# Performance work log

Measured on AMD Instinct MI355X. Metric: run time of the kernel, lower is better.

The kernel has to match this reference:

```python
import jax, jax.numpy as jnp
import numpy as np


def setup_inputs() -> dict:
    key0 = jax.random.key(0)
    ks = jax.random.split(key0, 7)
    B, N, M, D, H = 2, 1024, 1024, 256, 128
    s = 1.0 / np.sqrt(D)
    return {
        "query": jax.random.normal(ks[0], (B, N, D), dtype=jnp.float32),
        "key": jax.random.normal(ks[1], (B, M, D), dtype=jnp.float32),
        "Wa_w": jax.random.normal(ks[2], (D, H), dtype=jnp.float32) * s,
        "Wa_b": jax.random.normal(ks[3], (H,), dtype=jnp.float32) * 0.02,
        "Wb_w": jax.random.normal(ks[4], (D, H), dtype=jnp.float32) * s,
        "Wb_b": jax.random.normal(ks[5], (H,), dtype=jnp.float32) * 0.02,
        "v_w": jax.random.normal(ks[6], (H,), dtype=jnp.float32) / np.sqrt(H),
    }


def reference(query, key, Wa_w, Wa_b, Wb_w, Wb_b, v_w):
    # a: [B,N,H], b: [B,M,H]
    a = query @ Wa_w + Wa_b
    b = key @ Wb_w + Wb_b
    # scores: tanh of broadcast add [B,N,M,H], contracted with v -> [B,N,M]
    scores = jnp.einsum("bnmh,h->bnm", jnp.tanh(a[:, :, None, :] + b[:, None, :, :]), v_w)
    attn = jax.nn.softmax(scores, axis=-1)
    # attended: [B,N,D]
    return jnp.einsum("bnm,bmd->bnd", attn, key)
```

## Files before the change

kernel.cpp:

```cpp
#include <hip/hip_runtime.h>
#include <hip/hip_fp16.h>

#define BB 2
#define NN 1024
#define MM 1024
#define DD 256
#define HH 128
#define C2LE 2.8853900817779268f
#define NEG2LOG2E -2.8853900817779268f
#define SHIFT_C -4.3280860f

typedef float v2f __attribute__((ext_vector_type(2)));
typedef float v4f __attribute__((ext_vector_type(4)));
typedef _Float16 h8 __attribute__((ext_vector_type(8)));

__global__ __launch_bounds__(256) void proj_conv_kernel(
    const float* __restrict__ query, const float* __restrict__ key,
    const float* __restrict__ Wa_w, const float* __restrict__ Wa_b,
    const float* __restrict__ Wb_w, const float* __restrict__ Wb_b,
    float* __restrict__ EaT, float* __restrict__ Eb,
    __half* __restrict__ KT_hi) {
    __shared__ float rows[8][DD];
    __shared__ float partial[8][HH];
    __shared__ float t[64][65];
    const int tid = threadIdx.x;

    if (blockIdx.x >= 512) {
        const int cid = blockIdx.x - 512;
        const int m0 = (cid & 15) * 64, d0 = ((cid >> 4) & 3) * 64, b = cid >> 6;
        for (int i = tid; i < 1024; i += 256) {
            const int r = i >> 4, c4 = i & 15;
            const float4 v =
                *(const float4*)&key[((size_t)(b * MM + m0 + r)) * DD + d0 + c4 * 4];
            t[r][c4 * 4 + 0] = v.x; t[r][c4 * 4 + 1] = v.y;
            t[r][c4 * 4 + 2] = v.z; t[r][c4 * 4 + 3] = v.w;
        }
        __syncthreads();
        for (int i = tid; i < 4096; i += 256) {
            const int dr = i >> 6, mc = i & 63;
            KT_hi[((size_t)(b * DD + d0 + dr)) * MM + m0 + mc] =
                __float2half(t[mc][dr]);
        }
        return;
    }

    const int rb = blockIdx.x * 8;
    const bool isA = rb < BB * NN;
    const float* in = isA ? query : key;
    const float* W  = isA ? Wa_w : Wb_w;
    const float* bias = isA ? Wa_b : Wb_b;
    const int base = isA ? rb : rb - BB * NN;

    const float4* in4 = (const float4*)(in + (size_t)base * DD);
    float4* rows4 = (float4*)rows;
    rows4[tid] = in4[tid];
    rows4[tid + 256] = in4[tid + 256];
    __syncthreads();

    const int h = tid & 127, half = tid >> 7;
    const int d0 = half * 128;
    float acc[8] = {};
    for (int d = d0; d < d0 + 128; d += 4) {
        const float w0 = W[(d + 0) * HH + h];
        const float w1 = W[(d + 1) * HH + h];
        const float w2 = W[(d + 2) * HH + h];
        const float w3 = W[(d + 3) * HH + h];
#pragma unroll
        for (int r = 0; r < 8; ++r) {
            const float4 rv = *(const float4*)&rows[r][d];
            acc[r] = fmaf(rv.x, w0, fmaf(rv.y, w1, fmaf(rv.z, w2, fmaf(rv.w, w3, acc[r]))));
        }
    }
    if (half) {
#pragma unroll
        for (int r = 0; r < 8; ++r) partial[r][h] = acc[r];
    }
    __syncthreads();
    if (!half) {
        const float bv = bias[h];
        float ev[8];
#pragma unroll
        for (int r = 0; r < 8; ++r)
            ev[r] = __builtin_amdgcn_exp2f(C2LE * (acc[r] + partial[r][h] + bv));
        if (isA) {
            const int bq = base >> 10, nb = base & (NN - 1);
            float* dst = EaT + ((size_t)(bq * HH + h)) * NN + nb;
            *(float4*)dst = *(float4*)&ev[0];
            *(float4*)(dst + 4) = *(float4*)&ev[4];
        } else {
#pragma unroll
            for (int r = 0; r < 8; ++r)
                Eb[(size_t)(base + r) * HH + h] = ev[r];
        }
    }
}

__global__ __launch_bounds__(256) void scores_kernel(
    const float* __restrict__ EaT, const float* __restrict__ Eb,
    const float* __restrict__ v_w, __half* __restrict__ Ph,
    float* __restrict__ psum) {
    __shared__ float b_s[128 * 64];
    __shared__ float a_s[64 * 32];
    const int tid = threadIdx.x;
    const int m0 = blockIdx.x * 128, n0 = blockIdx.y * 32, b = blockIdx.z;
    const int lane = tid & 63;
    const int ng = __builtin_amdgcn_readfirstlane(threadIdx.x >> 6);
    const int skey = lane & 15;

    v2f acc[2][4] = {};
    for (int hc = 0; hc < 2; ++hc) {
        __syncthreads();
        for (int i = tid; i < 128 * 16; i += 256) {
            const int r = i >> 4, h4 = i & 15;
            *(float4*)&b_s[r * 64 + ((h4 ^ (r & 15)) << 2)] =
                *(const float4*)&Eb[((size_t)(b * MM + m0 + r)) * HH + hc * 64 + h4 * 4];
        }
        for (int i = tid; i < 64 * 8; i += 256) {
            const int hh = i >> 3, n4 = i & 7;
            *(float4*)&a_s[hh * 32 + n4 * 4] =
                *(const float4*)&EaT[((size_t)(b * HH + hc * 64 + hh)) * NN + n0 + n4 * 4];
        }
        __syncthreads();

#pragma unroll 4
        for (int h4 = 0; h4 < 16; ++h4) {
            const float4 w4 = *(const float4*)&v_w[hc * 64 + h4 * 4];
            const float* ap = &a_s[h4 * 4 * 32 + ng * 8];
            v2f A0[4], A1[4], A2[4], A3[4];
#pragma unroll
            for (int np = 0; np < 4; ++np) {
                A0[np] = *(const v2f*)&ap[0 * 32 + np * 2];
                A1[np] = *(const v2f*)&ap[1 * 32 + np * 2];
                A2[np] = *(const v2f*)&ap[2 * 32 + np * 2];
                A3[np] = *(const v2f*)&ap[3 * 32 + np * 2];
            }
#pragma unroll
            for (int mt = 0; mt < 2; ++mt) {
                const float4 b4 = *(const float4*)
                    &b_s[(mt * 64 + lane) * 64 + ((h4 ^ skey) << 2)];
#pragma unroll
                for (int np = 0; np < 4; ++np) {
                    const v2f u0 = A0[np] * b4.x + 1.0f;
                    const v2f u1 = A1[np] * b4.y + 1.0f;
                    const v2f u2 = A2[np] * b4.z + 1.0f;
                    const v2f u3 = A3[np] * b4.w + 1.0f;
                    const v2f p01 = u0 * u1, p23 = u2 * u3;
                    const v2f An = w4.x * u1 + w4.y * u0;
                    const v2f Bn = w4.z * u3 + w4.w * u2;
                    const v2f num = An * p23 + Bn * p01;
                    const v2f Pp = p01 * p23;
                    v2f r2;
                    r2.x = __builtin_amdgcn_rcpf(Pp.x);
                    r2.y = __builtin_amdgcn_rcpf(Pp.y);
                    acc[mt][np] = num * r2 + acc[mt][np];
                }
            }
        }
    }

    const size_t prow = ((size_t)b * NN + n0 + ng * 8) * MM + m0 + lane;
#pragma unroll
    for (int j = 0; j < 8; ++j) {
#pragma unroll
        for (int mt = 0; mt < 2; ++mt) {
            const float pv = __builtin_amdgcn_exp2f(
                fmaf(acc[mt][j >> 1][j & 1], NEG2LOG2E, SHIFT_C));
            Ph[prow + (size_t)j * MM + mt * 64] = __float2half(pv);
            float s = pv;
#pragma unroll
            for (int o = 32; o > 0; o >>= 1) s += __shfl_xor(s, o);
            if (lane == 0)
                psum[((size_t)(m0 / 64 + mt) * BB + b) * NN + n0 + ng * 8 + j] = s;
        }
    }
}

__global__ __launch_bounds__(512) void attend_kernel(
    const __half* __restrict__ Ph, const __half* __restrict__ KT_hi,
    float* __restrict__ partial) {
    __shared__ __align__(16) __half Ab[2][4096];
    __shared__ __align__(16) __half Bh[2][4096];

    const int bid = blockIdx.x;
    const int xcd = bid & 7, idx = bid >> 3;
    const int b = idx & 1, ks = (idx >> 1) & 3, dt = (idx >> 3) & 3;
    const int nt = xcd * 2 + ((idx >> 5) & 1);
    const int n0 = nt * 64, d0 = dt * 64, m0 = ks * 256;

    const int tid = threadIdx.x;
    const int lane = tid & 63;
    const int srow = tid & 15, skg = (tid >> 4) & 3;
    const int ssub = tid >> 6, skh = ssub & 1, st = ssub >> 1;
    const int scol = m0 + skh * 32 + skg * 8;

    const __half* srcA = Ph    + ((size_t)(b * NN + n0 + st * 16 + srow)) * MM + scol;
    const __half* srcB = KT_hi + ((size_t)(b * DD + d0 + st * 16 + srow)) * MM + scol;

    const int wave = __builtin_amdgcn_readfirstlane(threadIdx.x >> 6);
    const int t0 = (wave >> 2) * 2, td = wave & 3;

    v4f c0 = {0.f, 0.f, 0.f, 0.f}, c1 = c0;

    h8 ra = *(const h8*)srcA;
    h8 rb = *(const h8*)srcB;

    int cur = 0;
#pragma unroll 1
    for (int step = 0; step < 4; ++step) {
        *(h8*)&Ab[cur][tid * 8] = ra;
        *(h8*)&Bh[cur][tid * 8] = rb;
        if (step < 3) {
            ra = *(const h8*)(srcA + (step + 1) * 64);
            rb = *(const h8*)(srcB + (step + 1) * 64);
        }
        asm volatile("s_waitcnt lgkmcnt(0)" ::: "memory");
        __builtin_amdgcn_sched_barrier(0);
        __builtin_amdgcn_s_barrier();

        const __half* A = Ab[cur];
        const __half* B = Bh[cur];
        const h8 a00 = *(const h8*)&A[((t0 * 2 + 0) * 64 + lane) * 8];
        const h8 a01 = *(const h8*)&A[((t0 * 2 + 1) * 64 + lane) * 8];
        const h8 a10 = *(const h8*)&A[((t0 * 2 + 2) * 64 + lane) * 8];
        const h8 a11 = *(const h8*)&A[((t0 * 2 + 3) * 64 + lane) * 8];
        const h8 b0  = *(const h8*)&B[((td * 2 + 0) * 64 + lane) * 8];
        const h8 b1  = *(const h8*)&B[((td * 2 + 1) * 64 + lane) * 8];
        c0 = __builtin_amdgcn_mfma_f32_16x16x32_f16(a00, b0, c0, 0, 0, 0);
        c0 = __builtin_amdgcn_mfma_f32_16x16x32_f16(a01, b1, c0, 0, 0, 0);
        c1 = __builtin_amdgcn_mfma_f32_16x16x32_f16(a10, b0, c1, 0, 0, 0);
        c1 = __builtin_amdgcn_mfma_f32_16x16x32_f16(a11, b1, c1, 0, 0, 0);
        cur ^= 1;
    }

    const int row16 = lane & 15, kg = lane >> 4;
    float* pp0 = partial +
        (((size_t)ks * BB + b) * NN + n0 + t0 * 16 + kg * 4) * DD + d0 + td * 16 + row16;
    float* pp1 = pp0 + (size_t)16 * DD;
#pragma unroll
    for (int r = 0; r < 4; ++r) pp0[(size_t)r * DD] = c0[r];
#pragma unroll
    for (int r = 0; r < 4; ++r) pp1[(size_t)r * DD] = c1[r];
}

__global__ __launch_bounds__(256) void combine_kernel(
    const float* __restrict__ partial, const float* __restrict__ psum,
    float* __restrict__ out) {
    const int n = blockIdx.x, b = blockIdx.y, d = threadIdx.x;
    float s = 0.f;
#pragma unroll
    for (int q = 0; q < 16; ++q)
        s += psum[((size_t)q * BB + b) * NN + n];
    const size_t off = ((size_t)b * NN + n) * DD + d;
    float a = 0.f;
#pragma unroll
    for (int ks = 0; ks < 4; ++ks)
        a += partial[((size_t)ks * BB) * NN * DD + off];
    out[off] = a * __builtin_amdgcn_rcpf(s);
}

extern "C" void kernel_launch(void* const* d_in, const int* in_sizes, int n_in,
                              void* d_out, int out_size, void* d_ws, size_t ws_size,
                              hipStream_t stream) {
    const float* query = (const float*)d_in[0];
    const float* key   = (const float*)d_in[1];
    const float* Wa_w  = (const float*)d_in[2];
    const float* Wa_b  = (const float*)d_in[3];
    const float* Wb_w  = (const float*)d_in[4];
    const float* Wb_b  = (const float*)d_in[5];
    const float* v_w   = (const float*)d_in[6];
    float* out = (float*)d_out;

    float* ws = (float*)d_ws;
    float* EaT  = ws;
    float* Eb   = EaT + BB * NN * HH;
    float* psum = Eb + BB * MM * HH;
    __half* Ph    = (__half*)(psum + 16 * BB * NN);
    __half* KT_hi = Ph + (size_t)BB * NN * MM;
    float* partial = (float*)(KT_hi + (size_t)BB * DD * MM);

    proj_conv_kernel<<<dim3(512 + 128), dim3(256), 0, stream>>>(
        query, key, Wa_w, Wa_b, Wb_w, Wb_b, EaT, Eb, KT_hi);
    scores_kernel<<<dim3(MM / 128, NN / 32, BB), dim3(256), 0, stream>>>(
        EaT, Eb, v_w, Ph, psum);
    attend_kernel<<<dim3(512), dim3(512), 0, stream>>>(
        Ph, KT_hi, partial);
    combine_kernel<<<dim3(NN, BB), dim3(256), 0, stream>>>(
        partial, psum, out);
}
```

Measured before the change: 58.31 us.

## Fuse combine into attend kernel by removing split-K over M

```diff
diff --git a/kernel.cpp b/kernel.cpp
--- a/kernel.cpp
+++ b/kernel.cpp
@@ -177,85 +177,74 @@
 
 __global__ __launch_bounds__(512) void attend_kernel(
     const __half* __restrict__ Ph, const __half* __restrict__ KT_hi,
-    float* __restrict__ partial) {
-    __shared__ __align__(16) __half Ab[2][4096];
-    __shared__ __align__(16) __half Bh[2][4096];
+    const float* __restrict__ psum, float* __restrict__ out) {
+    __shared__ __align__(16) __half Ab[2][4 * 512];
+    __shared__ __align__(16) __half Bb[2][8 * 512];
+    __shared__ float inv[32];
 
     const int bid = blockIdx.x;
-    const int xcd = bid & 7, idx = bid >> 3;
-    const int b = idx & 1, ks = (idx >> 1) & 3, dt = (idx >> 3) & 3;
-    const int nt = xcd * 2 + ((idx >> 5) & 1);
-    const int n0 = nt * 64, d0 = dt * 64, m0 = ks * 256;
+    const int g = bid & 7, nt = bid >> 3;
+    const int dt = g >> 1, b = g & 1;
+    const int n0 = nt * 32, d0 = dt * 64;
 
     const int tid = threadIdx.x;
     const int lane = tid & 63;
-    const int srow = tid & 15, skg = (tid >> 4) & 3;
-    const int ssub = tid >> 6, skh = ssub & 1, st = ssub >> 1;
-    const int scol = m0 + skh * 32 + skg * 8;
-
-    const __half* srcA = Ph    + ((size_t)(b * NN + n0 + st * 16 + srow)) * MM + scol;
-    const __half* srcB = KT_hi + ((size_t)(b * DD + d0 + st * 16 + srow)) * MM + scol;
+    const int row16 = lane & 15, kg = lane >> 4;
+
+    if (tid < 32) {
+        float s = 0.f;
+#pragma unroll
+        for (int q = 0; q < 16; ++q)
+            s += psum[((size_t)q * BB + b) * NN + n0 + tid];
+        inv[tid] = __builtin_amdgcn_rcpf(s);
+    }
+
+    const int cb = tid >> 6;
+    const int sdB = cb >> 1, skhB = cb & 1;
+    const __half* srcB = KT_hi +
+        ((size_t)(b * DD + d0 + sdB * 16 + row16)) * MM + skhB * 32 + kg * 8;
+    const bool hasA = tid < 256;
+    const int ca = cb & 3;
+    const int snA = ca >> 1, skhA = ca & 1;
+    const __half* srcA = Ph +
+        ((size_t)(b * NN + n0 + snA * 16 + row16)) * MM + skhA * 32 + kg * 8;
 
     const int wave = __builtin_amdgcn_readfirstlane(threadIdx.x >> 6);
-    const int t0 = (wave >> 2) * 2, td = wave & 3;
-
-    v4f c0 = {0.f, 0.f, 0.f, 0.f}, c1 = c0;
-
-    h8 ra = *(const h8*)srcA;
+    const int t = wave >> 2, td = wave & 3;
+
+    v4f c = {0.f, 0.f, 0.f, 0.f};
+
     h8 rb = *(const h8*)srcB;
+    h8 ra;
+    if (hasA) ra = *(const h8*)srcA;
 
     int cur = 0;
 #pragma unroll 1
-    for (int step = 0; step < 4; ++step) {
-        *(h8*)&Ab[cur][tid * 8] = ra;
-        *(h8*)&Bh[cur][tid * 8] = rb;
-        if (step < 3) {
-            ra = *(const h8*)(srcA + (step + 1) * 64);
+    for (int step = 0; step < 16; ++step) {
+        *(h8*)&Bb[cur][cb * 512 + lane * 8] = rb;
+        if (hasA) *(h8*)&Ab[cur][ca * 512 + lane * 8] = ra;
+        if (step < 15) {
             rb = *(const h8*)(srcB + (step + 1) * 64);
+            if (hasA) ra = *(const h8*)(srcA + (step + 1) * 64);
         }
         asm volatile("s_waitcnt lgkmcnt(0)" ::: "memory");
         __builtin_amdgcn_sched_barrier(0);
         __builtin_amdgcn_s_barrier();
 
-        const __half* A = Ab[cur];
-        const __half* B = Bh[cur];
-        const h8 a00 = *(const h8*)&A[((t0 * 2 + 0) * 64 + lane) * 8];
-        const h8 a01 = *(const h8*)&A[((t0 * 2 + 1) * 64 + lane) * 8];
-        const h8 a10 = *(const h8*)&A[((t0 * 2 + 2) * 64 + lane) * 8];
-        const h8 a11 = *(const h8*)&A[((t0 * 2 + 3) * 64 + lane) * 8];
-        const h8 b0  = *(const h8*)&B[((td * 2 + 0) * 64 + lane) * 8];
-        const h8 b1  = *(const h8*)&B[((td * 2 + 1) * 64 + lane) * 8];
-        c0 = __builtin_amdgcn_mfma_f32_16x16x32_f16(a00, b0, c0, 0, 0, 0);
-        c0 = __builtin_amdgcn_mfma_f32_16x16x32_f16(a01, b1, c0, 0, 0, 0);
-        c1 = __builtin_amdgcn_mfma_f32_16x16x32_f16(a10, b0, c1, 0, 0, 0);
-        c1 = __builtin_amdgcn_mfma_f32_16x16x32_f16(a11, b1, c1, 0, 0, 0);
+        const h8 a0 = *(const h8*)&Ab[cur][(t * 2 + 0) * 512 + lane * 8];
+        const h8 a1 = *(const h8*)&Ab[cur][(t * 2 + 1) * 512 + lane * 8];
+        const h8 b0 = *(const h8*)&Bb[cur][(td * 2 + 0) * 512 + lane * 8];
+        const h8 b1 = *(const h8*)&Bb[cur][(td * 2 + 1) * 512 + lane * 8];
+        c = __builtin_amdgcn_mfma_f32_16x16x32_f16(a0, b0, c, 0, 0, 0);
+        c = __builtin_amdgcn_mfma_f32_16x16x32_f16(a1, b1, c, 0, 0, 0);
         cur ^= 1;
     }
 
-    const int row16 = lane & 15, kg = lane >> 4;
-    float* pp0 = partial +
-        (((size_t)ks * BB + b) * NN + n0 + t0 * 16 + kg * 4) * DD + d0 + td * 16 + row16;
-    float* pp1 = pp0 + (size_t)16 * DD;
-#pragma unroll
-    for (int r = 0; r < 4; ++r) pp0[(size_t)r * DD] = c0[r];
-#pragma unroll
-    for (int r = 0; r < 4; ++r) pp1[(size_t)r * DD] = c1[r];
-}
-
-__global__ __launch_bounds__(256) void combine_kernel(
-    const float* __restrict__ partial, const float* __restrict__ psum,
-    float* __restrict__ out) {
-    const int n = blockIdx.x, b = blockIdx.y, d = threadIdx.x;
-    float s = 0.f;
-#pragma unroll
-    for (int q = 0; q < 16; ++q)
-        s += psum[((size_t)q * BB + b) * NN + n];
-    const size_t off = ((size_t)b * NN + n) * DD + d;
-    float a = 0.f;
-#pragma unroll
-    for (int ks = 0; ks < 4; ++ks)
-        a += partial[((size_t)ks * BB) * NN * DD + off];
-    out[off] = a * __builtin_amdgcn_rcpf(s);
+    const int nloc = t * 16 + kg * 4;
+    float* po = out + ((size_t)(b * NN + n0 + nloc)) * DD + d0 + td * 16 + row16;
+#pragma unroll
+    for (int r = 0; r < 4; ++r)
+        po[(size_t)r * DD] = c[r] * inv[nloc + r];
 }
 
 extern "C" void kernel_launch(void* const* d_in, const int* in_sizes, int n_in,
@@ -276,14 +265,11 @@
     float* psum = Eb + BB * MM * HH;
     __half* Ph    = (__half*)(psum + 16 * BB * NN);
     __half* KT_hi = Ph + (size_t)BB * NN * MM;
-    float* partial = (float*)(KT_hi + (size_t)BB * DD * MM);
 
     proj_conv_kernel<<<dim3(512 + 128), dim3(256), 0, stream>>>(
         query, key, Wa_w, Wa_b, Wb_w, Wb_b, EaT, Eb, KT_hi);
     scores_kernel<<<dim3(MM / 128, NN / 32, BB), dim3(256), 0, stream>>>(
         EaT, Eb, v_w, Ph, psum);
-    attend_kernel<<<dim3(512), dim3(512), 0, stream>>>(
-        Ph, KT_hi, partial);
-    combine_kernel<<<dim3(NN, BB), dim3(256), 0, stream>>>(
-        partial, psum, out);
-}
+    attend_kernel<<<dim3(256), dim3(512), 0, stream>>>(
+        Ph, KT_hi, psum, out);
+}
```

Result: faster. 57.14 us (-2.0%).
